# Optimization experiments

Measured on AMD Instinct MI355X. Metric: run time of the kernel, lower is better.

The kernel has to match this reference:

```python
import jax, jax.numpy as jnp
import numpy as np

B, N, S = 2, 16384, 4096
C_FEAT = 6
RADII = (0.5, 1.0)
NSAMPLES = (16, 32)
MLPS = ([9, 16, 16, 32], [9, 32, 32, 64])  # in-channels = 3 (xyz) + 6 (features)
IC, PC, OUT = 64, 96, 128  # image ch, point ch (32+64), fusion out
RC = PC // 4


def _w(key, o, i):
    return jax.random.normal(key, (o, i), jnp.float32) / np.sqrt(i)


def setup_inputs() -> dict:
    key = jax.random.key(0)
    ks = jax.random.split(key, 40)
    inp = {
        "xyz": jax.random.normal(ks[0], (B, N, 3), jnp.float32),
        "features": jax.random.normal(ks[1], (B, C_FEAT, N), jnp.float32),
        "img_features": jax.random.normal(ks[2], (B, IC, S), jnp.float32),
    }
    k = 3
    for s, mlp in enumerate(MLPS):
        for l in range(len(mlp) - 1):
            inp[f"w{s}_{l}"] = _w(ks[k], mlp[l + 1], mlp[l]); k += 1
            inp[f"b{s}_{l}"] = jnp.zeros((mlp[l + 1],), jnp.float32)
    inp["w_img"] = _w(ks[k], PC, IC); k += 1
    inp["b_img"] = jnp.zeros((PC,), jnp.float32)
    inp["w_fc2"] = _w(ks[k], RC, PC); k += 1
    inp["b_fc2"] = jnp.zeros((RC,), jnp.float32)
    inp["w_fc3"] = _w(ks[k], 1, RC); k += 1
    inp["b_fc3"] = jnp.zeros((1,), jnp.float32)
    inp["w_pc"] = _w(ks[k], PC, PC); k += 1
    inp["b_pc"] = jnp.zeros((PC,), jnp.float32)
    inp["w_fuse"] = _w(ks[k], OUT, 2 * PC); k += 1
    inp["b_fuse"] = jnp.zeros((OUT,), jnp.float32)
    return inp


def conv1d(w, b, x):
    # 1x1 Conv1d: w [O,C], x [B,C,N]
    return jnp.einsum('oc,bcn->bon', w, x) + b[None, :, None]


def fps(xyz, npoint):
    # farthest point sampling. xyz: [B,N,3] -> idx [B,npoint]
    b, n, _ = xyz.shape
    first = jnp.zeros((b,), jnp.int32)

    def body(carry, _):
        dists, last = carry
        last_xyz = jnp.take_along_axis(xyz, last[:, None, None].astype(jnp.int32), axis=1)  # [B,1,3]
        d = jnp.sum((xyz - last_xyz) ** 2, -1)  # [B,N]
        dists = jnp.minimum(dists, d)
        nxt = jnp.argmax(dists, -1).astype(jnp.int32)
        return (dists, nxt), nxt

    (_, _), rest = jax.lax.scan(body, (jnp.full((b, n), 1e10, jnp.float32), first), None, length=npoint - 1)
    return jnp.concatenate([first[None, :], rest], 0).T  # [B,npoint]


def ball_query(xyz, new_xyz, radius, nsample):
    # xyz [B,N,3], new_xyz [B,S,3] -> idx [B,S,nsample]
    d2 = jnp.sum((new_xyz[:, :, None, :] - xyz[:, None, :, :]) ** 2, -1)  # [B,S,N]
    ar = jnp.arange(xyz.shape[1], dtype=jnp.int32)
    keys = jnp.where(d2 < radius * radius, ar[None, None, :], xyz.shape[1])
    idx = -jax.lax.top_k(-keys, nsample)[0]  # nsample smallest keys (first in-ball indices)
    first = idx[..., :1]
    idx = jnp.where(idx == xyz.shape[1], first, idx)  # pad with first in-ball index (pointnet2 semantics)
    return jnp.minimum(idx, xyz.shape[1] - 1)


def _forward(xyz, features, img_features, params):
    (w0_0, b0_0, w0_1, b0_1, w0_2, b0_2,
     w1_0, b1_0, w1_1, b1_1, w1_2, b1_2,
     w_img, b_img, w_fc2, b_fc2, w_fc3, b_fc3, w_pc, b_pc, w_fuse, b_fuse) = params
    layers = [[(w0_0, b0_0), (w0_1, b0_1), (w0_2, b0_2)],
              [(w1_0, b1_0), (w1_1, b1_1), (w1_2, b1_2)]]

    fps_idx = fps(xyz, S)  # [B,S]
    new_xyz = jnp.take_along_axis(xyz, fps_idx[:, :, None], axis=1)  # [B,S,3]

    outs = []
    for radius, nsample, mlp in zip(RADII, NSAMPLES, layers):
        idx = ball_query(xyz, new_xyz, radius, nsample)  # [B,S,K]
        g_xyz = jax.vmap(lambda p, i: p[i])(xyz, idx)  # [B,S,K,3]
        g_xyz = (g_xyz - new_xyz[:, :, None, :]).transpose(0, 3, 1, 2)  # [B,3,S,K]
        g_feat = jax.vmap(lambda f, i: f[:, i])(features, idx)  # [B,C,S,K]
        h = jnp.concatenate([g_xyz, g_feat], axis=1)  # [B,3+C,S,K]  (use_xyz)
        for w, b in mlp:
            h = jax.nn.relu(jnp.einsum('oc,bcsk->bosk', w, h) + b[None, :, None, None])
        outs.append(jnp.max(h, axis=-1))  # max-pool over neighborhood -> [B,Cout,S]
    point_feats = jnp.concatenate(outs, axis=1)  # [B,96,S]

    # IA_Layer (BatchNorm at default running stats ~ identity; omitted)
    img = jax.nn.relu(conv1d(w_img, b_img, img_features))  # [B,PC,S]
    flat = img.transpose(0, 2, 1)  # [B,S,PC]
    ri = jnp.tanh(flat @ w_fc2.T + b_fc2)  # [B,S,RC]
    att = jax.nn.sigmoid(ri @ w_fc3.T + b_fc3).transpose(0, 2, 1)  # [B,1,S]
    img_r = img + img * att
    img_new = jax.nn.relu(conv1d(w_pc, b_pc, img_r))  # [B,PC,S]

    fused = jnp.concatenate([point_feats, img_new], axis=1)  # [B,2*PC,S]
    return jax.nn.relu(conv1d(w_fuse, b_fuse, fused))  # [B,OUT,S]


def reference(xyz, features, img_features,
              w0_0, b0_0, w0_1, b0_1, w0_2, b0_2,
              w1_0, b1_0, w1_1, b1_1, w1_2, b1_2,
              w_img, b_img, w_fc2, b_fc2, w_fc3, b_fc3,
              w_pc, b_pc, w_fuse, b_fuse):
    params = (w0_0, b0_0, w0_1, b0_1, w0_2, b0_2,
              w1_0, b1_0, w1_1, b1_1, w1_2, b1_2,
              w_img, b_img, w_fc2, b_fc2, w_fc3, b_fc3, w_pc, b_pc, w_fuse, b_fuse)
    return _forward(xyz, features, img_features, params)
```

## Files before the change

### kernel.cpp

```cpp
#include <hip/hip_runtime.h>
#include <cstdint>

typedef unsigned long long u64;
typedef float v2f __attribute__((ext_vector_type(2)));

static constexpr int BB = 2;
static constexpr int NN = 16384;
static constexpr int SS = 4096;

template <int CTRL>
__device__ __forceinline__ u64 dpp_max_step(u64 k) {
  int lo = (int)(unsigned)(k & 0xffffffffull);
  int hi = (int)(unsigned)(k >> 32);
  int slo = __builtin_amdgcn_update_dpp(0, lo, CTRL, 0xF, 0xF, true);
  int shi = __builtin_amdgcn_update_dpp(0, hi, CTRL, 0xF, 0xF, true);
  u64 o = ((u64)(unsigned)shi << 32) | (u64)(unsigned)slo;
  return (o > k) ? o : k;
}

__device__ __forceinline__ unsigned wave_umax_bcast(unsigned v) {
  unsigned o;
#define WSTEP(C)                                                              \
  o = (unsigned)__builtin_amdgcn_update_dpp(0, (int)v, C, 0xF, 0xF, true);   \
  v = (o > v) ? o : v;
  WSTEP(0x111)
  WSTEP(0x112)
  WSTEP(0x114)
  WSTEP(0x118)
  WSTEP(0x142)
  WSTEP(0x143)
#undef WSTEP
  return (unsigned)__builtin_amdgcn_readlane((int)v, 63);
}

__device__ __forceinline__ v2f emin2(v2f a, v2f b) {
  v2f r; r[0] = fminf(a[0], b[0]); r[1] = fminf(a[1], b[1]); return r;
}
__device__ __forceinline__ v2f emax2(v2f a, v2f b) {
  v2f r; r[0] = fmaxf(a[0], b[0]); r[1] = fmaxf(a[1], b[1]); return r;
}

__device__ __forceinline__ unsigned spread4(unsigned v) {
  return (v & 1u) | ((v & 2u) << 2) | ((v & 4u) << 4) | ((v & 8u) << 6);
}

__device__ __forceinline__ unsigned cell_of(float x, float y, float z) {
  int cx = (int)floorf((x + 4.f) * 2.f);
  int cy = (int)floorf((y + 4.f) * 2.f);
  int cz = (int)floorf((z + 4.f) * 2.f);
  cx = min(max(cx, 0), 15); cy = min(max(cy, 0), 15); cz = min(max(cz, 0), 15);
  return spread4((unsigned)cx) | (spread4((unsigned)cy) << 1) |
         (spread4((unsigned)cz) << 2);
}

__global__ __launch_bounds__(1024) void sort_kernel(
    const float* __restrict__ xyz, float4* __restrict__ spts)
{
  const int b = blockIdx.x;
  const float* X = xyz + (size_t)b * NN * 3;
  float4* SP = spts + (size_t)b * NN;
  const int t = threadIdx.x;
  const int lane = t & 63, wid = t >> 6;

  __shared__ unsigned h[4096];
  __shared__ unsigned wtot[16];
  for (int j = t; j < 4096; j += 1024) h[j] = 0;
  __syncthreads();

  for (int i = 0; i < 16; ++i) {
    int p = i * 1024 + t;
    atomicAdd(&h[cell_of(X[p * 3 + 0], X[p * 3 + 1], X[p * 3 + 2])], 1u);
  }
  __syncthreads();

  unsigned a0 = h[4 * t], a1 = h[4 * t + 1], a2 = h[4 * t + 2], a3 = h[4 * t + 3];
  unsigned s4 = a0 + a1 + a2 + a3;
  unsigned incl = s4;
  for (int off = 1; off < 64; off <<= 1) {
    unsigned v = (unsigned)__shfl_up((int)incl, off);
    if (lane >= off) incl += v;
  }
  if (lane == 63) wtot[wid] = incl;
  __syncthreads();
  if (t == 0) {
    unsigned run = 0;
    for (int j = 0; j < 16; ++j) { unsigned tm = wtot[j]; wtot[j] = run; run += tm; }
  }
  __syncthreads();
  unsigned ex = wtot[wid] + (incl - s4);
  h[4 * t] = ex; h[4 * t + 1] = ex + a0;
  h[4 * t + 2] = ex + a0 + a1; h[4 * t + 3] = ex + a0 + a1 + a2;
  __syncthreads();

  for (int i = 0; i < 16; ++i) {
    int p = i * 1024 + t;
    float x = X[p * 3 + 0], y = X[p * 3 + 1], z = X[p * 3 + 2];
    unsigned pos = atomicAdd(&h[cell_of(x, y, z)], 1u);
    SP[pos] = make_float4(x, y, z, __int_as_float(p));
  }
}

__global__ __launch_bounds__(512, 2) void fps_kernel(
    const float* __restrict__ xyz, const float4* __restrict__ spts,
    float* __restrict__ new_xyz)
{
#pragma clang fp contract(off)
  const int b = blockIdx.x;
  const float* X = xyz + (size_t)b * NN * 3;
  float* NX = new_xyz + (size_t)b * SS * 3;
  const float4* SP = spts + (size_t)b * NN;
  const int t = threadIdx.x;
  const int lane = t & 63, wid = t >> 6;
  const float4* WP = SP + wid * 2048;

  v2f xp0, xp1, xp2, xp3, xp4, xp5, xp6, xp7,
      xp8, xp9, xp10, xp11, xp12, xp13, xp14, xp15;
  v2f yp0, yp1, yp2, yp3, yp4, yp5, yp6, yp7,
      yp8, yp9, yp10, yp11, yp12, yp13, yp14, yp15;
  v2f zp0, zp1, zp2, zp3, zp4, zp5, zp6, zp7,
      zp8, zp9, zp10, zp11, zp12, zp13, zp14, zp15;
  v2f dp0, dp1, dp2, dp3, dp4, dp5, dp6, dp7,
      dp8, dp9, dp10, dp11, dp12, dp13, dp14, dp15;
  unsigned na0, na1, na2, na3, na4, na5, na6, na7,
           na8, na9, na10, na11, na12, na13, na14, na15;
  unsigned nb0, nb1, nb2, nb3, nb4, nb5, nb6, nb7,
           nb8, nb9, nb10, nb11, nb12, nb13, nb14, nb15;

#define LOADV(v)                                                              \
  {                                                                           \
    float4 Pa = WP[(2 * (v)) * 64 + lane];                                    \
    float4 Pb = WP[(2 * (v) + 1) * 64 + lane];                                \
    xp##v[0] = Pa.x; xp##v[1] = Pb.x;                                         \
    yp##v[0] = Pa.y; yp##v[1] = Pb.y;                                         \
    zp##v[0] = Pa.z; zp##v[1] = Pb.z;                                         \
    na##v = ~__float_as_uint(Pa.w); nb##v = ~__float_as_uint(Pb.w);           \
    dp##v[0] = 1e10f; dp##v[1] = 1e10f;                                       \
  }
  LOADV(0)  LOADV(1)  LOADV(2)  LOADV(3)
  LOADV(4)  LOADV(5)  LOADV(6)  LOADV(7)
  LOADV(8)  LOADV(9)  LOADV(10) LOADV(11)
  LOADV(12) LOADV(13) LOADV(14) LOADV(15)
#undef LOADV

  float bnx = 0.f, bny = 0.f, bnz = 0.f, bxx = 0.f, bxy = 0.f, bxz = 0.f;
#define SUBBOX(J, A, B)                                                       \
  {                                                                           \
    v2f nv = emin2(xp##A, xp##B), xv = emax2(xp##A, xp##B);                   \
    float mnx = fminf(nv[0], nv[1]), mxx = fmaxf(xv[0], xv[1]);               \
    nv = emin2(yp##A, yp##B); xv = emax2(yp##A, yp##B);                       \
    float mny = fminf(nv[0], nv[1]), mxy = fmaxf(xv[0], xv[1]);               \
    nv = emin2(zp##A, zp##B); xv = emax2(zp##A, zp##B);                       \
    float mnz = fminf(nv[0], nv[1]), mxz = fmaxf(xv[0], xv[1]);               \
    for (int off = 1; off < 64; off <<= 1) {                                  \
      mnx = fminf(mnx, __shfl_xor(mnx, off));                                 \
      mxx = fmaxf(mxx, __shfl_xor(mxx, off));                                 \
      mny = fminf(mny, __shfl_xor(mny, off));                                 \
      mxy = fmaxf(mxy, __shfl_xor(mxy, off));                                 \
      mnz = fminf(mnz, __shfl_xor(mnz, off));                                 \
      mxz = fmaxf(mxz, __shfl_xor(mxz, off));                                 \
    }                                                                         \
    if ((lane & 7) == J) { bnx = mnx; bny = mny; bnz = mnz;                   \
                           bxx = mxx; bxy = mxy; bxz = mxz; }                 \
  }
  SUBBOX(0, 0, 1)   SUBBOX(1, 2, 3)   SUBBOX(2, 4, 5)   SUBBOX(3, 6, 7)
  SUBBOX(4, 8, 9)   SUBBOX(5, 10, 11) SUBBOX(6, 12, 13) SUBBOX(7, 14, 15)
#undef SUBBOX

  unsigned wkhi = __float_as_uint(1e10f), wklo = 0u;

  __shared__ u64 s_part[2][8];
  int sel = 0;

  for (int it = 1; it < SS; ++it) {
    const float qx = X[sel * 3 + 0];
    const float qy = X[sel * 3 + 1];
    const float qz = X[sel * 3 + 2];
    if (t == 0) {
      NX[(it - 1) * 3 + 0] = qx;
      NX[(it - 1) * 3 + 1] = qy;
      NX[(it - 1) * 3 + 2] = qz;
    }
    v2f q2x, q2y, q2z;
    q2x[0] = qx; q2x[1] = qx;
    q2y[0] = qy; q2y[1] = qy;
    q2z[0] = qz; q2z[1] = qz;

    float tx = fmaxf(fmaxf(__fsub_rn(bnx, qx), __fsub_rn(qx, bxx)), 0.f);
    float ty = fmaxf(fmaxf(__fsub_rn(bny, qy), __fsub_rn(qy, bxy)), 0.f);
    float tz = fmaxf(fmaxf(__fsub_rn(bnz, qz), __fsub_rn(qz, bxz)), 0.f);
    float lb2 = fmaf(tx, tx, fmaf(ty, ty, __fmul_rn(tz, tz)));
    u64 bm = __ballot(__fmul_rn(lb2, 0.99998474f) < __uint_as_float(wkhi));
    unsigned m = (unsigned)bm & 0xFFu;

#define SUBUPD(J, A, B)                                                       \
    if (m & (1u << J)) {                                                      \
      v2f dxA = xp##A - q2x, dyA = yp##A - q2y, dzA = zp##A - q2z;            \
      v2f sA = (dxA * dxA + dyA * dyA) + dzA * dzA;                           \
      dp##A = emin2(dp##A, sA);                                               \
      v2f dxB = xp##B - q2x, dyB = yp##B - q2y, dzB = zp##B - q2z;            \
      v2f sB = (dxB * dxB + dyB * dyB) + dzB * dzB;                           \
      dp##B = emin2(dp##B, sB);                                               \
      v2f mv = emax2(dp##A, dp##B);                                           \
      unsigned mm = __float_as_uint(fmaxf(mv[0], mv[1]));                     \
      mm = wave_umax_bcast(mm);                                               \
      unsigned c0 = (__float_as_uint(dp##A[0]) == mm) ? na##A : 0u;           \
      unsigned c1 = (__float_as_uint(dp##A[1]) == mm) ? nb##A : 0u;           \
      unsigned c2 = (__float_as_uint(dp##B[0]) == mm) ? na##B : 0u;           \
      unsigned c3 = (__float_as_uint(dp##B[1]) == mm) ? nb##B : 0u;           \
      unsigned cc = wave_umax_bcast(max(max(c0, c1), max(c2, c3)));           \
      if ((lane & 7) == J) { wkhi = mm; wklo = cc; }                          \
    }
    SUBUPD(0, 0, 1)   SUBUPD(1, 2, 3)   SUBUPD(2, 4, 5)   SUBUPD(3, 6, 7)
    SUBUPD(4, 8, 9)   SUBUPD(5, 10, 11) SUBUPD(6, 12, 13) SUBUPD(7, 14, 15)
#undef SUBUPD

    u64 kw = ((u64)wkhi << 32) | (u64)wklo;
    kw = dpp_max_step<0x124>(kw);
    kw = dpp_max_step<0x122>(kw);
    kw = dpp_max_step<0x121>(kw);

    const int pb = it & 1;
    if (lane == 0) s_part[pb][wid] = kw;
    __syncthreads();
    u64 kk = s_part[pb][lane & 7];
    kk = dpp_max_step<0x124>(kk);
    kk = dpp_max_step<0x122>(kk);
    kk = dpp_max_step<0x121>(kk);
    sel = (int)(~(unsigned)(kk & 0xffffffffull));
    sel = __builtin_amdgcn_readfirstlane(sel);
  }
  if (t == 0) {
    NX[(SS - 1) * 3 + 0] = X[sel * 3 + 0];
    NX[(SS - 1) * 3 + 1] = X[sel * 3 + 1];
    NX[(SS - 1) * 3 + 2] = X[sel * 3 + 2];
  }
}

template <int NS>
__global__ __launch_bounds__(256) void ballq_kernel(
    const float* __restrict__ xyz, const float* __restrict__ new_xyz,
    int* __restrict__ out, float r2)
{
  const int q = blockIdx.x * 4 + (threadIdx.x >> 6);
  const int lane = threadIdx.x & 63;
  const int b = q >> 12;
  const float* X = xyz + (size_t)b * NN * 3;
  const float cx = new_xyz[q * 3 + 0];
  const float cy = new_xyz[q * 3 + 1];
  const float cz = new_xyz[q * 3 + 2];
  int* o = out + (size_t)q * NS;
  int base = 0;
  int firstIdx = 0x7fffffff;
  for (int c0 = 0; c0 < NN; c0 += 64) {
    const int p = c0 + lane;
    float dx = __fsub_rn(cx, X[p * 3 + 0]);
    float dy = __fsub_rn(cy, X[p * 3 + 1]);
    float dz = __fsub_rn(cz, X[p * 3 + 2]);
    float d2 = __fadd_rn(__fadd_rn(__fmul_rn(dx, dx), __fmul_rn(dy, dy)),
                         __fmul_rn(dz, dz));
    const bool inb = d2 < r2;
    const unsigned long long mm = __ballot(inb);
    if (inb) {
      int rank = base + (int)__popcll(mm & ((1ull << lane) - 1ull));
      if (rank < NS) {
        o[rank] = p;
        if (rank == 0) firstIdx = p;
      }
    }
    base += (int)__popcll(mm);
    if (base >= NS) break;
  }
#pragma unroll
  for (int off = 32; off >= 1; off >>= 1)
    firstIdx = min(firstIdx, __shfl_xor(firstIdx, off));
  for (int r = base + lane; r < NS; r += 64) o[r] = firstIdx;
}

template <int NS, int C1, int C2, int C3>
__global__ __launch_bounds__(256) void group_mlp_kernel(
    const float* __restrict__ xyz, const float* __restrict__ feat,
    const float* __restrict__ new_xyz, const int* __restrict__ idx,
    const float* __restrict__ w0, const float* __restrict__ b0,
    const float* __restrict__ w1, const float* __restrict__ b1,
    const float* __restrict__ w2, const float* __restrict__ b2,
    float* __restrict__ pf, int chOff)
{
  constexpr int QPB = 256 / NS;
  const int q = blockIdx.x * QPB + (int)(threadIdx.x / NS);
  const int k = (int)(threadIdx.x % NS);
  const int b = q >> 12;
  const int s = q & (SS - 1);
  const float* X = xyz + (size_t)b * NN * 3;
  const float* F = feat + (size_t)b * 6 * NN;
  const int p = idx[(size_t)q * NS + k];

  float in[9];
  in[0] = X[p * 3 + 0] - new_xyz[q * 3 + 0];
  in[1] = X[p * 3 + 1] - new_xyz[q * 3 + 1];
  in[2] = X[p * 3 + 2] - new_xyz[q * 3 + 2];
#pragma unroll
  for (int c = 0; c < 6; ++c) in[3 + c] = F[c * NN + p];

  float h1[C1];
#pragma unroll
  for (int oc = 0; oc < C1; ++oc) {
    float a = b0[oc];
#pragma unroll
    for (int c = 0; c < 9; ++c) a = fmaf(w0[oc * 9 + c], in[c], a);
    h1[oc] = fmaxf(a, 0.f);
  }
  float h2[C2];
#pragma unroll
  for (int oc = 0; oc < C2; ++oc) {
    float a = b1[oc];
#pragma unroll
    for (int c = 0; c < C1; ++c) a = fmaf(w1[oc * C1 + c], h1[c], a);
    h2[oc] = fmaxf(a, 0.f);
  }
#pragma unroll
  for (int oc = 0; oc < C3; ++oc) {
    float a = b2[oc];
#pragma unroll
    for (int c = 0; c < C2; ++c) a = fmaf(w2[oc * C2 + c], h2[c], a);
    float v = fmaxf(a, 0.f);
#pragma unroll
    for (int off = NS / 2; off >= 1; off >>= 1)
      v = fmaxf(v, __shfl_xor(v, off));
    if (k == 0) pf[(((size_t)b * 96) + chOff + oc) * SS + s] = v;
  }
}

__global__ __launch_bounds__(256) void img_fuse_kernel(
    const float* __restrict__ imgf, const float* __restrict__ pf,
    const float* __restrict__ w_img, const float* __restrict__ b_img,
    const float* __restrict__ w_fc2, const float* __restrict__ b_fc2,
    const float* __restrict__ w_fc3, const float* __restrict__ b_fc3,
    const float* __restrict__ w_pc, const float* __restrict__ b_pc,
    const float* __restrict__ w_fuse, const float* __restrict__ b_fuse,
    float* __restrict__ out)
{
  constexpr int TS = 32;
  __shared__ float x_lds[64][TS];
  __shared__ float img_lds[96][TS];
  __shared__ float ri_lds[24][TS];
  __shared__ float att_lds[TS];
  __shared__ float imgn_lds[96][TS];
  __shared__ float pf_lds[96][TS];

  const int blk = blockIdx.x;
  const int b = blk / (SS / TS);
  const int s0 = (blk % (SS / TS)) * TS;
  const int tid = threadIdx.x;

  for (int i = tid; i < 64 * TS; i += 256) {
    int c = i / TS, s = i % TS;
    x_lds[c][s] = imgf[((size_t)b * 64 + c) * SS + s0 + s];
  }
  for (int i = tid; i < 96 * TS; i += 256) {
    int c = i / TS, s = i % TS;
    pf_lds[c][s] = pf[((size_t)b * 96 + c) * SS + s0 + s];
  }
  __syncthreads();

  for (int i = tid; i < 96 * TS; i += 256) {
    int oc = i / TS, s = i % TS;
    float a = b_img[oc];
#pragma unroll
    for (int c = 0; c < 64; ++c) a = fmaf(w_img[oc * 64 + c], x_lds[c][s], a);
    img_lds[oc][s] = fmaxf(a, 0.f);
  }
  __syncthreads();

  for (int i = tid; i < 24 * TS; i += 256) {
    int r = i / TS, s = i % TS;
    float a = b_fc2[r];
#pragma unroll
    for (int c = 0; c < 96; ++c) a = fmaf(w_fc2[r * 96 + c], img_lds[c][s], a);
    ri_lds[r][s] = tanhf(a);
  }
  __syncthreads();

  if (tid < TS) {
    float a = b_fc3[0];
#pragma unroll
    for (int r = 0; r < 24; ++r) a = fmaf(w_fc3[r], ri_lds[r][tid], a);
    att_lds[tid] = 1.f / (1.f + expf(-a));
  }
  __syncthreads();

  for (int i = tid; i < 96 * TS; i += 256) {
    int c = i / TS, s = i % TS;
    float v = img_lds[c][s];
    img_lds[c][s] = fmaf(v, att_lds[s], v);
  }
  __syncthreads();

  for (int i = tid; i < 96 * TS; i += 256) {
    int oc = i / TS, s = i % TS;
    float a = b_pc[oc];
#pragma unroll
    for (int c = 0; c < 96; ++c) a = fmaf(w_pc[oc * 96 + c], img_lds[c][s], a);
    imgn_lds[oc][s] = fmaxf(a, 0.f);
  }
  __syncthreads();

  for (int i = tid; i < 128 * TS; i += 256) {
    int oc = i / TS, s = i % TS;
    float a = b_fuse[oc];
#pragma unroll
    for (int c = 0; c < 96; ++c) a = fmaf(w_fuse[oc * 192 + c], pf_lds[c][s], a);
#pragma unroll
    for (int c = 0; c < 96; ++c) a = fmaf(w_fuse[oc * 192 + 96 + c], imgn_lds[c][s], a);
    out[((size_t)b * 128 + oc) * SS + s0 + s] = fmaxf(a, 0.f);
  }
}

extern "C" void kernel_launch(void* const* d_in, const int* in_sizes, int n_in,
                              void* d_out, int out_size, void* d_ws, size_t ws_size,
                              hipStream_t stream)
{
  const float* xyz    = (const float*)d_in[0];
  const float* feat   = (const float*)d_in[1];
  const float* imgf   = (const float*)d_in[2];
  const float* w0_0   = (const float*)d_in[3];
  const float* b0_0   = (const float*)d_in[4];
  const float* w0_1   = (const float*)d_in[5];
  const float* b0_1   = (const float*)d_in[6];
  const float* w0_2   = (const float*)d_in[7];
  const float* b0_2   = (const float*)d_in[8];
  const float* w1_0   = (const float*)d_in[9];
  const float* b1_0   = (const float*)d_in[10];
  const float* w1_1   = (const float*)d_in[11];
  const float* b1_1   = (const float*)d_in[12];
  const float* w1_2   = (const float*)d_in[13];
  const float* b1_2   = (const float*)d_in[14];
  const float* w_img  = (const float*)d_in[15];
  const float* b_img  = (const float*)d_in[16];
  const float* w_fc2  = (const float*)d_in[17];
  const float* b_fc2  = (const float*)d_in[18];
  const float* w_fc3  = (const float*)d_in[19];
  const float* b_fc3  = (const float*)d_in[20];
  const float* w_pc   = (const float*)d_in[21];
  const float* b_pc   = (const float*)d_in[22];
  const float* w_fuse = (const float*)d_in[23];
  const float* b_fuse = (const float*)d_in[24];
  float* out = (float*)d_out;

  float4* spts = (float4*)d_ws;
  float*  nxyz = (float*)(spts + (size_t)BB * NN);
  int*    idx0 = (int*)(nxyz + (size_t)BB * SS * 3);
  int*    idx1 = idx0 + (size_t)BB * SS * 16;
  float*  pf   = (float*)(idx1 + (size_t)BB * SS * 32);

  sort_kernel<<<BB, 1024, 0, stream>>>(xyz, spts);
  fps_kernel<<<BB, 512, 0, stream>>>(xyz, spts, nxyz);
  ballq_kernel<16><<<BB * SS / 4, 256, 0, stream>>>(xyz, nxyz, idx0, 0.25f);
  ballq_kernel<32><<<BB * SS / 4, 256, 0, stream>>>(xyz, nxyz, idx1, 1.0f);
  group_mlp_kernel<16, 16, 16, 32><<<BB * SS / 16, 256, 0, stream>>>(
      xyz, feat, nxyz, idx0, w0_0, b0_0, w0_1, b0_1, w0_2, b0_2, pf, 0);
  group_mlp_kernel<32, 32, 32, 64><<<BB * SS / 8, 256, 0, stream>>>(
      xyz, feat, nxyz, idx1, w1_0, b1_0, w1_1, b1_1, w1_2, b1_2, pf, 32);
  img_fuse_kernel<<<BB * SS / 32, 256, 0, stream>>>(
      imgf, pf, w_img, b_img, w_fc2, b_fc2, w_fc3, b_fc3, w_pc, b_pc,
      w_fuse, b_fuse, out);
}
```

Measured before the change: 5.189 ms.

## Widen FPS to 1024 threads with per-wave bounding box culling and float4 xyz copy

FPS blocks grow from 512 to 1024 threads, so each wave holds 16 points per lane instead of 32, and the eight per-wave sub-boxes collapse into one wave-level bounding box with a single culling test and one update path. The sort kernel also writes a padded float4 copy of xyz, so each FPS iteration fetches the selected point with one vector load. The aim is to shorten the serial per-iteration critical path through more parallel lanes and fewer cross-lane reductions. The trade-off is coarser culling, since one box per wave skips work less often than eight sub-boxes, plus a 16-entry cross-wave reduction and extra workspace memory.

New measurement: 4.214 ms. -18.8%, faster.

```diff
diff --git a/kernel.cpp b/kernel.cpp
--- a/kernel.cpp
+++ b/kernel.cpp
@@ -21,7 +21,7 @@
 __device__ __forceinline__ unsigned wave_umax_bcast(unsigned v) {
   unsigned o;
 #define WSTEP(C)                                                              \
-  o = (unsigned)__builtin_amdgcn_update_dpp(0, (int)v, C, 0xF, 0xF, true);   \
+  o = (unsigned)__builtin_amdgcn_update_dpp(0, (int)v, C, 0xF, 0xF, true);    \
   v = (o > v) ? o : v;
   WSTEP(0x111)
   WSTEP(0x112)
@@ -54,11 +54,13 @@
 }
 
 __global__ __launch_bounds__(1024) void sort_kernel(
-    const float* __restrict__ xyz, float4* __restrict__ spts)
+    const float* __restrict__ xyz, float4* __restrict__ spts,
+    float4* __restrict__ x4)
 {
   const int b = blockIdx.x;
   const float* X = xyz + (size_t)b * NN * 3;
   float4* SP = spts + (size_t)b * NN;
+  float4* XO = x4 + (size_t)b * NN;
   const int t = threadIdx.x;
   const int lane = t & 63, wid = t >> 6;
 
@@ -69,7 +71,9 @@
 
   for (int i = 0; i < 16; ++i) {
     int p = i * 1024 + t;
-    atomicAdd(&h[cell_of(X[p * 3 + 0], X[p * 3 + 1], X[p * 3 + 2])], 1u);
+    float x = X[p * 3 + 0], y = X[p * 3 + 1], z = X[p * 3 + 2];
+    XO[p] = make_float4(x, y, z, 0.f);
+    atomicAdd(&h[cell_of(x, y, z)], 1u);
   }
   __syncthreads();
 
@@ -100,32 +104,24 @@
   }
 }
 
-__global__ __launch_bounds__(512, 2) void fps_kernel(
-    const float* __restrict__ xyz, const float4* __restrict__ spts,
+__global__ __launch_bounds__(1024) void fps_kernel(
+    const float4* __restrict__ x4, const float4* __restrict__ spts,
     float* __restrict__ new_xyz)
 {
 #pragma clang fp contract(off)
   const int b = blockIdx.x;
-  const float* X = xyz + (size_t)b * NN * 3;
+  const float4* XO = x4 + (size_t)b * NN;
   float* NX = new_xyz + (size_t)b * SS * 3;
-  const float4* SP = spts + (size_t)b * NN;
   const int t = threadIdx.x;
   const int lane = t & 63, wid = t >> 6;
-  const float4* WP = SP + wid * 2048;
-
-  v2f xp0, xp1, xp2, xp3, xp4, xp5, xp6, xp7,
-      xp8, xp9, xp10, xp11, xp12, xp13, xp14, xp15;
-  v2f yp0, yp1, yp2, yp3, yp4, yp5, yp6, yp7,
-      yp8, yp9, yp10, yp11, yp12, yp13, yp14, yp15;
-  v2f zp0, zp1, zp2, zp3, zp4, zp5, zp6, zp7,
-      zp8, zp9, zp10, zp11, zp12, zp13, zp14, zp15;
-  v2f dp0, dp1, dp2, dp3, dp4, dp5, dp6, dp7,
-      dp8, dp9, dp10, dp11, dp12, dp13, dp14, dp15;
-  unsigned na0, na1, na2, na3, na4, na5, na6, na7,
-           na8, na9, na10, na11, na12, na13, na14, na15;
-  unsigned nb0, nb1, nb2, nb3, nb4, nb5, nb6, nb7,
-           nb8, nb9, nb10, nb11, nb12, nb13, nb14, nb15;
-
+  const float4* WP = spts + (size_t)b * NN + wid * 1024;
+
+  v2f xp0, xp1, xp2, xp3, xp4, xp5, xp6, xp7;
+  v2f yp0, yp1, yp2, yp3, yp4, yp5, yp6, yp7;
+  v2f zp0, zp1, zp2, zp3, zp4, zp5, zp6, zp7;
+  v2f dp0, dp1, dp2, dp3, dp4, dp5, dp6, dp7;
+  unsigned na0, na1, na2, na3, na4, na5, na6, na7;
+  unsigned nb0, nb1, nb2, nb3, nb4, nb5, nb6, nb7;
 #define LOADV(v)                                                              \
   {                                                                           \
     float4 Pa = WP[(2 * (v)) * 64 + lane];                                    \
@@ -136,103 +132,95 @@
     na##v = ~__float_as_uint(Pa.w); nb##v = ~__float_as_uint(Pb.w);           \
     dp##v[0] = 1e10f; dp##v[1] = 1e10f;                                       \
   }
-  LOADV(0)  LOADV(1)  LOADV(2)  LOADV(3)
-  LOADV(4)  LOADV(5)  LOADV(6)  LOADV(7)
-  LOADV(8)  LOADV(9)  LOADV(10) LOADV(11)
-  LOADV(12) LOADV(13) LOADV(14) LOADV(15)
+  LOADV(0) LOADV(1) LOADV(2) LOADV(3) LOADV(4) LOADV(5) LOADV(6) LOADV(7)
 #undef LOADV
 
-  float bnx = 0.f, bny = 0.f, bnz = 0.f, bxx = 0.f, bxy = 0.f, bxz = 0.f;
-#define SUBBOX(J, A, B)                                                       \
-  {                                                                           \
-    v2f nv = emin2(xp##A, xp##B), xv = emax2(xp##A, xp##B);                   \
-    float mnx = fminf(nv[0], nv[1]), mxx = fmaxf(xv[0], xv[1]);               \
-    nv = emin2(yp##A, yp##B); xv = emax2(yp##A, yp##B);                       \
-    float mny = fminf(nv[0], nv[1]), mxy = fmaxf(xv[0], xv[1]);               \
-    nv = emin2(zp##A, zp##B); xv = emax2(zp##A, zp##B);                       \
-    float mnz = fminf(nv[0], nv[1]), mxz = fmaxf(xv[0], xv[1]);               \
-    for (int off = 1; off < 64; off <<= 1) {                                  \
-      mnx = fminf(mnx, __shfl_xor(mnx, off));                                 \
-      mxx = fmaxf(mxx, __shfl_xor(mxx, off));                                 \
-      mny = fminf(mny, __shfl_xor(mny, off));                                 \
-      mxy = fmaxf(mxy, __shfl_xor(mxy, off));                                 \
-      mnz = fminf(mnz, __shfl_xor(mnz, off));                                 \
-      mxz = fmaxf(mxz, __shfl_xor(mxz, off));                                 \
-    }                                                                         \
-    if ((lane & 7) == J) { bnx = mnx; bny = mny; bnz = mnz;                   \
-                           bxx = mxx; bxy = mxy; bxz = mxz; }                 \
-  }
-  SUBBOX(0, 0, 1)   SUBBOX(1, 2, 3)   SUBBOX(2, 4, 5)   SUBBOX(3, 6, 7)
-  SUBBOX(4, 8, 9)   SUBBOX(5, 10, 11) SUBBOX(6, 12, 13) SUBBOX(7, 14, 15)
-#undef SUBBOX
-
-  unsigned wkhi = __float_as_uint(1e10f), wklo = 0u;
-
-  __shared__ u64 s_part[2][8];
-  int sel = 0;
+  float bnx, bny, bnz, bxx, bxy, bxz;
+  {
+    v2f nx2 = emin2(emin2(emin2(xp0, xp1), emin2(xp2, xp3)),
+                    emin2(emin2(xp4, xp5), emin2(xp6, xp7)));
+    v2f xx2 = emax2(emax2(emax2(xp0, xp1), emax2(xp2, xp3)),
+                    emax2(emax2(xp4, xp5), emax2(xp6, xp7)));
+    v2f ny2 = emin2(emin2(emin2(yp0, yp1), emin2(yp2, yp3)),
+                    emin2(emin2(yp4, yp5), emin2(yp6, yp7)));
+    v2f xy2 = emax2(emax2(emax2(yp0, yp1), emax2(yp2, yp3)),
+                    emax2(emax2(yp4, yp5), emax2(yp6, yp7)));
+    v2f nz2 = emin2(emin2(emin2(zp0, zp1), emin2(zp2, zp3)),
+                    emin2(emin2(zp4, zp5), emin2(zp6, zp7)));
+    v2f xz2 = emax2(emax2(emax2(zp0, zp1), emax2(zp2, zp3)),
+                    emax2(emax2(zp4, zp5), emax2(zp6, zp7)));
+    bnx = fminf(nx2[0], nx2[1]); bxx = fmaxf(xx2[0], xx2[1]);
+    bny = fminf(ny2[0], ny2[1]); bxy = fmaxf(xy2[0], xy2[1]);
+    bnz = fminf(nz2[0], nz2[1]); bxz = fmaxf(xz2[0], xz2[1]);
+#pragma unroll
+    for (int off = 1; off < 64; off <<= 1) {
+      bnx = fminf(bnx, __shfl_xor(bnx, off));
+      bxx = fmaxf(bxx, __shfl_xor(bxx, off));
+      bny = fminf(bny, __shfl_xor(bny, off));
+      bxy = fmaxf(bxy, __shfl_xor(bxy, off));
+      bnz = fminf(bnz, __shfl_xor(bnz, off));
+      bxz = fmaxf(bxz, __shfl_xor(bxz, off));
+    }
+  }
+
+  unsigned wmaxb = __float_as_uint(1e10f), wni = 0u;
+
+  __shared__ u64 sp[2][16];
+  float qx, qy, qz;
+  { float4 q0 = XO[0]; qx = q0.x; qy = q0.y; qz = q0.z; }
 
   for (int it = 1; it < SS; ++it) {
-    const float qx = X[sel * 3 + 0];
-    const float qy = X[sel * 3 + 1];
-    const float qz = X[sel * 3 + 2];
     if (t == 0) {
       NX[(it - 1) * 3 + 0] = qx;
       NX[(it - 1) * 3 + 1] = qy;
       NX[(it - 1) * 3 + 2] = qz;
     }
-    v2f q2x, q2y, q2z;
-    q2x[0] = qx; q2x[1] = qx;
-    q2y[0] = qy; q2y[1] = qy;
-    q2z[0] = qz; q2z[1] = qz;
-
     float tx = fmaxf(fmaxf(__fsub_rn(bnx, qx), __fsub_rn(qx, bxx)), 0.f);
     float ty = fmaxf(fmaxf(__fsub_rn(bny, qy), __fsub_rn(qy, bxy)), 0.f);
     float tz = fmaxf(fmaxf(__fsub_rn(bnz, qz), __fsub_rn(qz, bxz)), 0.f);
     float lb2 = fmaf(tx, tx, fmaf(ty, ty, __fmul_rn(tz, tz)));
-    u64 bm = __ballot(__fmul_rn(lb2, 0.99998474f) < __uint_as_float(wkhi));
-    unsigned m = (unsigned)bm & 0xFFu;
-
-#define SUBUPD(J, A, B)                                                       \
-    if (m & (1u << J)) {                                                      \
-      v2f dxA = xp##A - q2x, dyA = yp##A - q2y, dzA = zp##A - q2z;            \
-      v2f sA = (dxA * dxA + dyA * dyA) + dzA * dzA;                           \
-      dp##A = emin2(dp##A, sA);                                               \
-      v2f dxB = xp##B - q2x, dyB = yp##B - q2y, dzB = zp##B - q2z;            \
-      v2f sB = (dxB * dxB + dyB * dyB) + dzB * dzB;                           \
-      dp##B = emin2(dp##B, sB);                                               \
-      v2f mv = emax2(dp##A, dp##B);                                           \
-      unsigned mm = __float_as_uint(fmaxf(mv[0], mv[1]));                     \
-      mm = wave_umax_bcast(mm);                                               \
-      unsigned c0 = (__float_as_uint(dp##A[0]) == mm) ? na##A : 0u;           \
-      unsigned c1 = (__float_as_uint(dp##A[1]) == mm) ? nb##A : 0u;           \
-      unsigned c2 = (__float_as_uint(dp##B[0]) == mm) ? na##B : 0u;           \
-      unsigned c3 = (__float_as_uint(dp##B[1]) == mm) ? nb##B : 0u;           \
-      unsigned cc = wave_umax_bcast(max(max(c0, c1), max(c2, c3)));           \
-      if ((lane & 7) == J) { wkhi = mm; wklo = cc; }                          \
+    if (__fmul_rn(lb2, 0.99998474f) < __uint_as_float(wmaxb)) {
+      v2f q2x, q2y, q2z;
+      q2x[0] = qx; q2x[1] = qx;
+      q2y[0] = qy; q2y[1] = qy;
+      q2z[0] = qz; q2z[1] = qz;
+#define UPDV(v)                                                               \
+      {                                                                       \
+        v2f dx = xp##v - q2x, dy = yp##v - q2y, dz = zp##v - q2z;             \
+        v2f s = (dx * dx + dy * dy) + dz * dz;                                \
+        dp##v = emin2(dp##v, s);                                              \
+      }
+      UPDV(0) UPDV(1) UPDV(2) UPDV(3) UPDV(4) UPDV(5) UPDV(6) UPDV(7)
+#undef UPDV
+      v2f mall = emax2(emax2(emax2(dp0, dp1), emax2(dp2, dp3)),
+                       emax2(emax2(dp4, dp5), emax2(dp6, dp7)));
+      unsigned mm = wave_umax_bcast(__float_as_uint(fmaxf(mall[0], mall[1])));
+      unsigned c = 0u;
+#define CSEL(v)                                                               \
+      c = max(c, (__float_as_uint(dp##v[0]) == mm) ? na##v : 0u);             \
+      c = max(c, (__float_as_uint(dp##v[1]) == mm) ? nb##v : 0u);
+      CSEL(0) CSEL(1) CSEL(2) CSEL(3) CSEL(4) CSEL(5) CSEL(6) CSEL(7)
+#undef CSEL
+      wni = wave_umax_bcast(c);
+      wmaxb = mm;
     }
-    SUBUPD(0, 0, 1)   SUBUPD(1, 2, 3)   SUBUPD(2, 4, 5)   SUBUPD(3, 6, 7)
-    SUBUPD(4, 8, 9)   SUBUPD(5, 10, 11) SUBUPD(6, 12, 13) SUBUPD(7, 14, 15)
-#undef SUBUPD
-
-    u64 kw = ((u64)wkhi << 32) | (u64)wklo;
-    kw = dpp_max_step<0x124>(kw);
-    kw = dpp_max_step<0x122>(kw);
-    kw = dpp_max_step<0x121>(kw);
-
     const int pb = it & 1;
-    if (lane == 0) s_part[pb][wid] = kw;
+    if (lane == 0) sp[pb][wid] = ((u64)wmaxb << 32) | (u64)wni;
     __syncthreads();
-    u64 kk = s_part[pb][lane & 7];
+    u64 kk = sp[pb][lane & 15];
+    kk = dpp_max_step<0x128>(kk);
     kk = dpp_max_step<0x124>(kk);
     kk = dpp_max_step<0x122>(kk);
     kk = dpp_max_step<0x121>(kk);
-    sel = (int)(~(unsigned)(kk & 0xffffffffull));
-    sel = __builtin_amdgcn_readfirstlane(sel);
+    unsigned widx = ~(unsigned)(kk & 0xffffffffull);
+    widx = (unsigned)__builtin_amdgcn_readfirstlane((int)widx);
+    float4 q = XO[widx];
+    qx = q.x; qy = q.y; qz = q.z;
   }
   if (t == 0) {
-    NX[(SS - 1) * 3 + 0] = X[sel * 3 + 0];
-    NX[(SS - 1) * 3 + 1] = X[sel * 3 + 1];
-    NX[(SS - 1) * 3 + 2] = X[sel * 3 + 2];
+    NX[(SS - 1) * 3 + 0] = qx;
+    NX[(SS - 1) * 3 + 1] = qy;
+    NX[(SS - 1) * 3 + 2] = qz;
   }
 }
 
@@ -447,13 +435,14 @@
   float* out = (float*)d_out;
 
   float4* spts = (float4*)d_ws;
-  float*  nxyz = (float*)(spts + (size_t)BB * NN);
+  float4* x4   = spts + (size_t)BB * NN;
+  float*  nxyz = (float*)(x4 + (size_t)BB * NN);
   int*    idx0 = (int*)(nxyz + (size_t)BB * SS * 3);
   int*    idx1 = idx0 + (size_t)BB * SS * 16;
   float*  pf   = (float*)(idx1 + (size_t)BB * SS * 32);
 
-  sort_kernel<<<BB, 1024, 0, stream>>>(xyz, spts);
-  fps_kernel<<<BB, 512, 0, stream>>>(xyz, spts, nxyz);
+  sort_kernel<<<BB, 1024, 0, stream>>>(xyz, spts, x4);
+  fps_kernel<<<BB, 1024, 0, stream>>>(x4, spts, nxyz);
   ballq_kernel<16><<<BB * SS / 4, 256, 0, stream>>>(xyz, nxyz, idx0, 0.25f);
   ballq_kernel<32><<<BB * SS / 4, 256, 0, stream>>>(xyz, nxyz, idx1, 1.0f);
   group_mlp_kernel<16, 16, 16, 32><<<BB * SS / 16, 256, 0, stream>>>(
```
